# Kernel optimization log

Hardware: AMD Instinct MI355X
Metric: run time of the kernel (lower is better)

Reference implementation:

```python
import jax, jax.numpy as jnp
import numpy as np

B, Q, H, NH, HD = 2, 1024, 2048, 16, 128
QKV_ALPHA = 1e-4   # W8A8B8O8Linear output scale (a)
QKV_BETA = 1.0     # W8A8B8O8Linear bias scale (b)
QK_SCALE = 1e-4    # BMM_S8T_S8N_F32T dequant scale
PV_SCALE = 2e-3    # BMM_S8T_S8N_S8T output scale
DENSE_ALPHA = 1e-5 # W8A8BFP32OFP32Linear dequant scale
INV_NORM = 1.0 / (HD ** 0.5)


def setup_inputs() -> dict:
    key = jax.random.key(0)
    ks = jax.random.split(key, 8)
    hidden_states = jax.random.randint(ks[0], (B, Q, H), -128, 128, dtype=jnp.int32)  # int8 activations
    residual = jax.random.normal(ks[1], (B, Q, H), dtype=jnp.float32)
    alibi = jax.random.normal(ks[2], (B * NH, 1, Q), dtype=jnp.float32) * 0.1
    causal = jnp.triu(jnp.ones((Q, Q), dtype=bool), k=1)  # True = masked (future positions)
    attention_mask = jnp.broadcast_to(causal[None, None], (B, 1, Q, Q))
    w_qkv = jax.random.randint(ks[3], (3 * H, H), -128, 128, dtype=jnp.int32)   # int8 weight
    b_qkv = jax.random.randint(ks[4], (3 * H,), -128, 128, dtype=jnp.int32)     # int8 bias
    w_dense = jax.random.randint(ks[5], (H, H), -128, 128, dtype=jnp.int32)     # int8 weight
    b_dense = jax.random.normal(ks[6], (H,), dtype=jnp.float32)                 # fp32 bias
    return dict(hidden_states=hidden_states, residual=residual, alibi=alibi,
                attention_mask=attention_mask, w_qkv=w_qkv, b_qkv=b_qkv,
                w_dense=w_dense, b_dense=b_dense)


def _quant_i8(x_f32):
    return jnp.clip(jnp.round(x_f32), -128, 127).astype(jnp.int32)


def reference(hidden_states, residual, alibi, attention_mask, w_qkv, b_qkv, w_dense, b_dense):
    # --- W8A8B8O8 fused QKV linear: int8 in, int8 out ---
    acc = jnp.einsum('bqh,oh->bqo', hidden_states, w_qkv)  # exact int32 accumulation
    fused_qkv = _quant_i8(acc.astype(jnp.float32) * QKV_ALPHA + b_qkv.astype(jnp.float32) * QKV_BETA)
    # _split_heads: [B,Q,3H] -> [B,Q,NH,3,HD]
    qkv = fused_qkv.reshape(B, Q, NH, 3, HD)
    q = qkv[..., 0, :].transpose(0, 2, 1, 3).reshape(B * NH, Q, HD)
    k = qkv[..., 1, :].transpose(0, 2, 1, 3).reshape(B * NH, Q, HD)
    v = qkv[..., 2, :].transpose(0, 2, 1, 3).reshape(B * NH, Q, HD)
    # --- BMM_S8T_S8N_F32T: int8 q @ k^T -> fp32 * scale, plus alibi bias ---
    scores_i32 = jnp.einsum('nqd,nkd->nqk', q, k)  # [B*NH,Q,KV] int32
    matmul_result = alibi * 1.0 + scores_i32.astype(jnp.float32) * QK_SCALE * INV_NORM
    attention_scores = matmul_result.reshape(B, NH, Q, Q)
    # masked softmax (True = masked)
    attn_weights = jnp.where(attention_mask, jnp.finfo(jnp.float32).min, attention_scores)
    attention_probs = jax.nn.softmax(attn_weights, axis=-1)
    # quantize probs to int8 with scale 1/127 (BMM_S8T_S8N_S8T A-side)
    p_i8 = _quant_i8(attention_probs * 127.0).reshape(B * NH, Q, Q)
    # --- BMM_S8T_S8N_S8T: int8 probs @ int8 v -> int8 context ---
    ctx_acc = jnp.einsum('nqk,nkd->nqd', p_i8, v)  # int32
    ctx_i8 = _quant_i8(ctx_acc.astype(jnp.float32) * PV_SCALE)
    # _merge_heads: [B*NH,Q,HD] -> [B,Q,H]
    ctx = ctx_i8.reshape(B, NH, Q, HD).transpose(0, 2, 1, 3).reshape(B, Q, H)
    # --- W8A8BFP32OFP32 dense: int8 in, fp32 out ---
    dense_acc = jnp.einsum('bqh,oh->bqo', ctx, w_dense)
    output = dense_acc.astype(jnp.float32) * DENSE_ALPHA + b_dense + residual
    return output
```

## Files before the change

kernel.cpp:

```cpp
#include <hip/hip_runtime.h>
#include <stdint.h>

typedef int i32x4 __attribute__((ext_vector_type(4)));

#define DEV __device__ __forceinline__

DEV void glds16(const void* g, void* l) {
  __builtin_amdgcn_global_load_lds(
      (const __attribute__((address_space(1))) void*)g,
      (__attribute__((address_space(3))) void*)l, 16, 0, 0);
}

DEV int clampi8(float f) {
  int v = (int)rintf(f);
  return v < -128 ? -128 : (v > 127 ? 127 : v);
}

__global__ void pack_all_kernel(const int* __restrict__ s0, const int* __restrict__ s1,
                                const int* __restrict__ s2, int8_t* __restrict__ d0,
                                int8_t* __restrict__ d1, int8_t* __restrict__ d2) {
  const int i = blockIdx.x * 256 + threadIdx.x;
  const int* s;
  int8_t* d;
  int j;
  if (i < 1048576) { s = s0; d = d0; j = i; }
  else if (i < 4194304) { s = s1; d = d1; j = i - 1048576; }
  else { s = s2; d = d2; j = i - 4194304; }
  int4 v = ((const int4*)s)[j];
  char4 c;
  c.x = (char)v.x; c.y = (char)v.y; c.z = (char)v.z; c.w = (char)v.w;
  ((char4*)d)[j] = c;
}

template<int K>
DEV void gemm_core(const int8_t* __restrict__ A, const int8_t* __restrict__ B,
                   int row0, int col0, i32x4 acc[4][4], char* lA, char* lB,
                   int l, int w, int wm, int wn) {
  const int lr = l & 15, lg = l >> 4;
  const int8_t* pA0 = A + (size_t)(row0 + (w * 2 + 0) * 16 + lr) * K + lg * 16;
  const int8_t* pA1 = A + (size_t)(row0 + (w * 2 + 1) * 16 + lr) * K + lg * 16;
  const int8_t* pB0 = B + (size_t)(col0 + (w * 2 + 0) * 16 + lr) * K + lg * 16;
  const int8_t* pB1 = B + (size_t)(col0 + (w * 2 + 1) * 16 + lr) * K + lg * 16;
  glds16(pA0, lA + (w * 2 + 0) * 1024);
  glds16(pA1, lA + (w * 2 + 1) * 1024);
  glds16(pB0, lB + (w * 2 + 0) * 1024);
  glds16(pB1, lB + (w * 2 + 1) * 1024);
  __syncthreads();
  int cur = 0;
  for (int k0 = 0; k0 < K; k0 += 64) {
    const int nxt = cur ^ 1;
    if (k0 + 64 < K) {
      glds16(pA0 + k0 + 64, lA + nxt * 8192 + (w * 2 + 0) * 1024);
      glds16(pA1 + k0 + 64, lA + nxt * 8192 + (w * 2 + 1) * 1024);
      glds16(pB0 + k0 + 64, lB + nxt * 8192 + (w * 2 + 0) * 1024);
      glds16(pB1 + k0 + 64, lB + nxt * 8192 + (w * 2 + 1) * 1024);
    }
    i32x4 a[4], b[4];
#pragma unroll
    for (int i = 0; i < 4; ++i)
      a[i] = *(const i32x4*)(lA + cur * 8192 + ((wm * 4 + i) * 64 + l) * 16);
#pragma unroll
    for (int j = 0; j < 4; ++j)
      b[j] = *(const i32x4*)(lB + cur * 8192 + ((wn * 4 + j) * 64 + l) * 16);
#pragma unroll
    for (int i = 0; i < 4; ++i)
#pragma unroll
      for (int j = 0; j < 4; ++j)
        acc[i][j] = __builtin_amdgcn_mfma_i32_16x16x64_i8(a[i], b[j], acc[i][j], 0, 0, 0);
    __syncthreads();
    cur = nxt;
  }
}

__global__ __launch_bounds__(256) void qkv_kernel(
    const int8_t* __restrict__ hs8, const int8_t* __restrict__ w8,
    const int* __restrict__ bq, int8_t* __restrict__ qb, int8_t* __restrict__ kb,
    int8_t* __restrict__ vT) {
  __shared__ __align__(16) char lA[16384];
  __shared__ __align__(16) char lB[16384];
  const int l = threadIdx.x & 63, w = threadIdx.x >> 6;
  const int wm = w >> 1, wn = w & 1;
  const int lr = l & 15, lg = l >> 4;
  const int row0 = blockIdx.y * 128, col0 = blockIdx.x * 128;
  i32x4 acc[4][4] = {};
  gemm_core<2048>(hs8, w8, row0, col0, acc, lA, lB, l, w, wm, wn);
#pragma unroll
  for (int j = 0; j < 4; ++j) {
    const int col = col0 + (wn * 4 + j) * 16 + lr;
    const float bias = (float)bq[col];
    const int nh = col / 384, rem = col - nh * 384;
    const int s = rem >> 7, d = rem & 127;
#pragma unroll
    for (int i = 0; i < 4; ++i) {
#pragma unroll
      for (int r = 0; r < 4; ++r) {
        const int row = row0 + (wm * 4 + i) * 16 + lg * 4 + r;
        const int bb = row >> 10, qpos = row & 1023;
        const int n = bb * 16 + nh;
        const int8_t c = (int8_t)clampi8((float)acc[i][j][r] * 1e-4f + bias);
        if (s == 0)      qb[((size_t)n << 17) + (qpos << 7) + d] = c;
        else if (s == 1) kb[((size_t)n << 17) + (qpos << 7) + d] = c;
        else             vT[((size_t)n << 17) + (d << 10) + qpos] = c;
      }
    }
  }
}

__global__ __launch_bounds__(256) void attn_stats_kernel(
    const int8_t* __restrict__ qb, const int8_t* __restrict__ kb,
    const float* __restrict__ alibi, float* __restrict__ stats) {
  const int n = blockIdx.y;
  const int tri = blockIdx.x;
  int qt = 0;
  while ((qt + 1) * (qt + 2) / 2 <= tri) ++qt;
  const int kt = tri - qt * (qt + 1) / 2;
  const int l = threadIdx.x & 63, w = threadIdx.x >> 6;
  const int lr = l & 15, lg = l >> 4;
  const int row0 = qt * 128;
  const int8_t* Qh = qb + ((size_t)n << 17);
  const int8_t* Kh = kb + ((size_t)n << 17);
  const float* al = alibi + n * 1024;

  i32x4 qa[2][2];
#pragma unroll
  for (int t = 0; t < 2; ++t)
#pragma unroll
    for (int ks = 0; ks < 2; ++ks)
      qa[t][ks] = *(const i32x4*)(Qh + (size_t)(row0 + (w * 2 + t) * 16 + lr) * 128 + ks * 64 + lg * 16);

  float sf[2][8][4];
#pragma unroll
  for (int nf = 0; nf < 8; ++nf) {
    const size_t krow = (size_t)(kt * 128 + nf * 16 + lr) * 128;
    const i32x4 bk0 = *(const i32x4*)(Kh + krow + lg * 16);
    const i32x4 bk1 = *(const i32x4*)(Kh + krow + 64 + lg * 16);
    const int col = kt * 128 + nf * 16 + lr;
    const float av = al[col];
#pragma unroll
    for (int t = 0; t < 2; ++t) {
      i32x4 sa = {0, 0, 0, 0};
      sa = __builtin_amdgcn_mfma_i32_16x16x64_i8(qa[t][0], bk0, sa, 0, 0, 0);
      sa = __builtin_amdgcn_mfma_i32_16x16x64_i8(qa[t][1], bk1, sa, 0, 0, 0);
#pragma unroll
      for (int r = 0; r < 4; ++r) {
        const int rowg = row0 + (w * 2 + t) * 16 + lg * 4 + r;
        sf[t][nf][r] = (col <= rowg)
            ? av + ((float)sa[r] * 1e-4f) * 0.08838834764831843f
            : -INFINITY;
      }
    }
  }
#pragma unroll
  for (int t = 0; t < 2; ++t)
#pragma unroll
    for (int r = 0; r < 4; ++r) {
      float tm = sf[t][0][r];
#pragma unroll
      for (int nf = 1; nf < 8; ++nf) tm = fmaxf(tm, sf[t][nf][r]);
#pragma unroll
      for (int o = 1; o < 16; o <<= 1) tm = fmaxf(tm, __shfl_xor(tm, o));
      float es = 0.f;
#pragma unroll
      for (int nf = 0; nf < 8; ++nf) es += __expf(sf[t][nf][r] - tm);
#pragma unroll
      for (int o = 1; o < 16; o <<= 1) es += __shfl_xor(es, o);
      if (lr == 0) {
        const int rowl = (w * 2 + t) * 16 + lg * 4 + r;
        float2* st = (float2*)stats;
        st[((n * 8 + qt) * 8 + kt) * 128 + rowl] = make_float2(tm, es);
      }
    }
}

__global__ __launch_bounds__(256) void attn_pv_kernel(
    const int8_t* __restrict__ qb, const int8_t* __restrict__ kb,
    const int8_t* __restrict__ vT, const float* __restrict__ alibi,
    const float* __restrict__ stats, int* __restrict__ slab0,
    int* __restrict__ slab1, int8_t* __restrict__ ctx) {
  __shared__ __align__(16) char lK[16384];
  __shared__ __align__(16) char lV[16384];
  __shared__ __align__(16) char lP[128 * 144];
  const int n = blockIdx.y, gi = blockIdx.x;
  const int sched[12] = {0x407, 0x847, 0x406, 0x403, 0x746, 0x305,
                         0x635, 0x304, 0x302, 0x534, 0x201, 0x100};
  const int s_ = sched[gi];
  const int qt = s_ & 15, kt0 = (s_ >> 4) & 15, kt1 = (s_ >> 8) & 15;
  const int l = threadIdx.x & 63, w = threadIdx.x >> 6;
  const int lr = l & 15, lg = l >> 4;
  const int row0 = qt * 128;
  const int8_t* Qh = qb + ((size_t)n << 17);
  const int8_t* Kh = kb + ((size_t)n << 17);
  const int8_t* Vh = vT + ((size_t)n << 17);
  const float* al = alibi + n * 1024;

  i32x4 qa[2][2];
#pragma unroll
  for (int t = 0; t < 2; ++t)
#pragma unroll
    for (int ks = 0; ks < 2; ++ks)
      qa[t][ks] = *(const i32x4*)(Qh + (size_t)(row0 + (w * 2 + t) * 16 + lr) * 128 + ks * 64 + lg * 16);

  float mrow[2][4], srow[2][4];
  const float2* st = (const float2*)stats;
#pragma unroll
  for (int t = 0; t < 2; ++t)
#pragma unroll
    for (int r = 0; r < 4; ++r) {
      const int rowl = (w * 2 + t) * 16 + lg * 4 + r;
      const int base = ((n * 8 + qt) * 8) * 128 + rowl;
      float m = -INFINITY;
      for (int k2 = 0; k2 <= qt; ++k2) m = fmaxf(m, st[base + k2 * 128].x);
      float s = 0.f;
      for (int k2 = 0; k2 <= qt; ++k2) {
        const float2 p = st[base + k2 * 128];
        s += p.y * __expf(p.x - m);
      }
      mrow[t][r] = m; srow[t][r] = s;
    }

  i32x4 pacc[2][8] = {};
  for (int kt = kt0; kt < kt1; ++kt) {
    __syncthreads();
#pragma unroll
    for (int e0 = 0; e0 < 4; ++e0) {
      const int e = w * 4 + e0, ks = e >> 3, mb = e & 7;
      glds16(Kh + (size_t)(kt * 128 + mb * 16 + lr) * 128 + ks * 64 + lg * 16, lK + e * 1024);
      glds16(Vh + (size_t)(mb * 16 + lr) * 1024 + kt * 128 + ks * 64 + lg * 16, lV + e * 1024);
    }
    __syncthreads();
#pragma unroll
    for (int nf = 0; nf < 8; ++nf) {
      const i32x4 bk0 = *(const i32x4*)(lK + nf * 1024 + l * 16);
      const i32x4 bk1 = *(const i32x4*)(lK + (8 + nf) * 1024 + l * 16);
      const int col = kt * 128 + nf * 16 + lr;
      const float av = al[col];
#pragma unroll
      for (int t = 0; t < 2; ++t) {
        i32x4 sa = {0, 0, 0, 0};
        sa = __builtin_amdgcn_mfma_i32_16x16x64_i8(qa[t][0], bk0, sa, 0, 0, 0);
        sa = __builtin_amdgcn_mfma_i32_16x16x64_i8(qa[t][1], bk1, sa, 0, 0, 0);
#pragma unroll
        for (int r = 0; r < 4; ++r) {
          const int rowl = (w * 2 + t) * 16 + lg * 4 + r;
          const int rowg = row0 + rowl;
          int p = 0;
          if (col <= rowg) {
            const float s = av + ((float)sa[r] * 1e-4f) * 0.08838834764831843f;
            p = (int)rintf(__expf(s - mrow[t][r]) / srow[t][r] * 127.0f);
          }
          lP[rowl * 144 + nf * 16 + lr] = (char)p;
        }
      }
    }
#pragma unroll
    for (int t = 0; t < 2; ++t) {
      const int rowl = (w * 2 + t) * 16 + lr;
      const i32x4 pa0 = *(const i32x4*)(lP + rowl * 144 + lg * 16);
      const i32x4 pa1 = *(const i32x4*)(lP + rowl * 144 + 64 + lg * 16);
#pragma unroll
      for (int nf = 0; nf < 8; ++nf) {
        const i32x4 vb0 = *(const i32x4*)(lV + nf * 1024 + l * 16);
        const i32x4 vb1 = *(const i32x4*)(lV + (8 + nf) * 1024 + l * 16);
        pacc[t][nf] = __builtin_amdgcn_mfma_i32_16x16x64_i8(pa0, vb0, pacc[t][nf], 0, 0, 0);
        pacc[t][nf] = __builtin_amdgcn_mfma_i32_16x16x64_i8(pa1, vb1, pacc[t][nf], 0, 0, 0);
      }
    }
  }
  const int bb = n >> 4, nh = n & 15;
  if (qt < 4) {
#pragma unroll
    for (int t = 0; t < 2; ++t)
#pragma unroll
      for (int nf = 0; nf < 8; ++nf)
#pragma unroll
        for (int r = 0; r < 4; ++r) {
          const int qpos = row0 + (w * 2 + t) * 16 + lg * 4 + r;
          const int d = nf * 16 + lr;
          ctx[((size_t)(bb * 1024 + qpos)) * 2048 + nh * 128 + d] =
              (int8_t)clampi8((float)pacc[t][nf][r] * 2e-3f);
        }
  } else {
    int* slab = kt0 ? slab1 : slab0;
#pragma unroll
    for (int t = 0; t < 2; ++t)
#pragma unroll
      for (int nf = 0; nf < 8; ++nf)
#pragma unroll
        for (int r = 0; r < 4; ++r) {
          const int qpos = row0 + (w * 2 + t) * 16 + lg * 4 + r;
          const int d = nf * 16 + lr;
          slab[(size_t)(bb * 512 + qpos - 512) * 2048 + nh * 128 + d] = pacc[t][nf][r];
        }
  }
}

__global__ void ctx_reduce_kernel(const int* __restrict__ slab0,
                                  const int* __restrict__ slab1,
                                  int8_t* __restrict__ ctx) {
  const int i = blockIdx.x * blockDim.x + threadIdx.x;
  const int4 a = ((const int4*)slab0)[i];
  const int4 b = ((const int4*)slab1)[i];
  const int elem0 = i * 4;
  const int r512 = elem0 >> 11, col = elem0 & 2047;
  const int bb = r512 >> 9, qpos = 512 + (r512 & 511);
  char4 c;
  c.x = (char)clampi8((float)(a.x + b.x) * 2e-3f);
  c.y = (char)clampi8((float)(a.y + b.y) * 2e-3f);
  c.z = (char)clampi8((float)(a.z + b.z) * 2e-3f);
  c.w = (char)clampi8((float)(a.w + b.w) * 2e-3f);
  ((char4*)ctx)[((size_t)(bb * 1024 + qpos) * 2048 + col) >> 2] = c;
}

__global__ __launch_bounds__(512, 1) void dense_kernel(
    const int8_t* __restrict__ c8, const int8_t* __restrict__ w8,
    const float* __restrict__ bd, const float* __restrict__ res,
    float* __restrict__ out) {
  __shared__ __align__(16) char lA[16384];
  __shared__ __align__(16) char lB[16384];
  const int l = threadIdx.x & 63, w = threadIdx.x >> 6;
  const int wm = w >> 2, wn = w & 3;
  const int lr = l & 15, lg = l >> 4;
  const int row0 = blockIdx.y * 128, col0 = blockIdx.x * 128;
  const int8_t* pA = c8 + (size_t)(row0 + w * 16 + lr) * 2048 + lg * 16;
  const int8_t* pB = w8 + (size_t)(col0 + w * 16 + lr) * 2048 + lg * 16;
  glds16(pA, lA + w * 1024);
  glds16(pB, lB + w * 1024);
  __syncthreads();
  i32x4 acc[4][2] = {};
  int cur = 0;
  for (int k0 = 0; k0 < 2048; k0 += 64) {
    const int nxt = cur ^ 1;
    if (k0 + 64 < 2048) {
      glds16(pA + k0 + 64, lA + nxt * 8192 + w * 1024);
      glds16(pB + k0 + 64, lB + nxt * 8192 + w * 1024);
    }
    i32x4 a[4], b[2];
#pragma unroll
    for (int i = 0; i < 4; ++i)
      a[i] = *(const i32x4*)(lA + cur * 8192 + ((wm * 4 + i) * 64 + l) * 16);
#pragma unroll
    for (int j = 0; j < 2; ++j)
      b[j] = *(const i32x4*)(lB + cur * 8192 + ((wn * 2 + j) * 64 + l) * 16);
#pragma unroll
    for (int i = 0; i < 4; ++i)
#pragma unroll
      for (int j = 0; j < 2; ++j)
        acc[i][j] = __builtin_amdgcn_mfma_i32_16x16x64_i8(a[i], b[j], acc[i][j], 0, 0, 0);
    __syncthreads();
    cur = nxt;
  }
#pragma unroll
  for (int j = 0; j < 2; ++j) {
    const int col = col0 + (wn * 2 + j) * 16 + lr;
    const float bias = bd[col];
#pragma unroll
    for (int i = 0; i < 4; ++i) {
#pragma unroll
      for (int r = 0; r < 4; ++r) {
        const int row = row0 + (wm * 4 + i) * 16 + lg * 4 + r;
        const size_t o = (size_t)row * 2048 + col;
        out[o] = (float)acc[i][j][r] * 1e-5f + bias + res[o];
      }
    }
  }
}

extern "C" void kernel_launch(void* const* d_in, const int* in_sizes, int n_in,
                              void* d_out, int out_size, void* d_ws, size_t ws_size,
                              hipStream_t stream) {
  const int* hs = (const int*)d_in[0];
  const float* res = (const float*)d_in[1];
  const float* alibi = (const float*)d_in[2];
  const int* wqkv = (const int*)d_in[4];
  const int* bqkv = (const int*)d_in[5];
  const int* wd = (const int*)d_in[6];
  const float* bd = (const float*)d_in[7];
  float* out = (float*)d_out;
  char* ws = (char*)d_ws;

  int8_t* hs8   = (int8_t*)(ws + 0);
  int8_t* wqkv8 = (int8_t*)(ws + 4194304);
  int*    slab0 = (int*)(ws + 0);
  int*    slab1 = (int*)(ws + 8388608);
  int8_t* wd8   = (int8_t*)(ws + 16777216);
  int8_t* q8b   = (int8_t*)(ws + 20971520);
  int8_t* k8b   = (int8_t*)(ws + 25165824);
  int8_t* vT8   = (int8_t*)(ws + 29360128);
  int8_t* ctx8  = (int8_t*)(ws + 33554432);
  float*  stats = (float*)(ws + 37748736);

  pack_all_kernel<<<20480, 256, 0, stream>>>(hs, wqkv, wd, hs8, wqkv8, wd8);
  qkv_kernel<<<dim3(48, 16), 256, 0, stream>>>(hs8, wqkv8, bqkv, q8b, k8b, vT8);
  attn_stats_kernel<<<dim3(36, 32), 256, 0, stream>>>(q8b, k8b, alibi, stats);
  attn_pv_kernel<<<dim3(12, 32), 256, 0, stream>>>(q8b, k8b, vT8, alibi, stats,
                                                   slab0, slab1, ctx8);
  ctx_reduce_kernel<<<2048, 256, 0, stream>>>(slab0, slab1, ctx8);
  dense_kernel<<<dim3(16, 16), 512, 0, stream>>>(ctx8, wd8, bd, res, out);
}
```

Measured before the change: 178.3 us.

## Load QKV GEMM operands directly into registers instead of staging through LDS

The QKV projection GEMM no longer stages A and B tiles through shared memory with global_load_lds. Each wave now loads its own MFMA fragments straight from global memory into registers, double-buffered across K steps. This removes the LDS writes and reads and the per-iteration __syncthreads barriers. In exchange, waves that share rows or columns of the tile load the same data separately, which adds cache traffic. The loads are also less coalesced, at 64-byte row segments.

```diff
diff --git a/kernel.cpp b/kernel.cpp
--- a/kernel.cpp
+++ b/kernel.cpp
@@ -32,58 +32,45 @@
   ((char4*)d)[j] = c;
 }
 
-template<int K>
-DEV void gemm_core(const int8_t* __restrict__ A, const int8_t* __restrict__ B,
-                   int row0, int col0, i32x4 acc[4][4], char* lA, char* lB,
-                   int l, int w, int wm, int wn) {
-  const int lr = l & 15, lg = l >> 4;
-  const int8_t* pA0 = A + (size_t)(row0 + (w * 2 + 0) * 16 + lr) * K + lg * 16;
-  const int8_t* pA1 = A + (size_t)(row0 + (w * 2 + 1) * 16 + lr) * K + lg * 16;
-  const int8_t* pB0 = B + (size_t)(col0 + (w * 2 + 0) * 16 + lr) * K + lg * 16;
-  const int8_t* pB1 = B + (size_t)(col0 + (w * 2 + 1) * 16 + lr) * K + lg * 16;
-  glds16(pA0, lA + (w * 2 + 0) * 1024);
-  glds16(pA1, lA + (w * 2 + 1) * 1024);
-  glds16(pB0, lB + (w * 2 + 0) * 1024);
-  glds16(pB1, lB + (w * 2 + 1) * 1024);
-  __syncthreads();
-  int cur = 0;
-  for (int k0 = 0; k0 < K; k0 += 64) {
-    const int nxt = cur ^ 1;
-    if (k0 + 64 < K) {
-      glds16(pA0 + k0 + 64, lA + nxt * 8192 + (w * 2 + 0) * 1024);
-      glds16(pA1 + k0 + 64, lA + nxt * 8192 + (w * 2 + 1) * 1024);
-      glds16(pB0 + k0 + 64, lB + nxt * 8192 + (w * 2 + 0) * 1024);
-      glds16(pB1 + k0 + 64, lB + nxt * 8192 + (w * 2 + 1) * 1024);
-    }
-    i32x4 a[4], b[4];
-#pragma unroll
-    for (int i = 0; i < 4; ++i)
-      a[i] = *(const i32x4*)(lA + cur * 8192 + ((wm * 4 + i) * 64 + l) * 16);
-#pragma unroll
-    for (int j = 0; j < 4; ++j)
-      b[j] = *(const i32x4*)(lB + cur * 8192 + ((wn * 4 + j) * 64 + l) * 16);
-#pragma unroll
-    for (int i = 0; i < 4; ++i)
-#pragma unroll
-      for (int j = 0; j < 4; ++j)
-        acc[i][j] = __builtin_amdgcn_mfma_i32_16x16x64_i8(a[i], b[j], acc[i][j], 0, 0, 0);
-    __syncthreads();
-    cur = nxt;
-  }
-}
-
 __global__ __launch_bounds__(256) void qkv_kernel(
     const int8_t* __restrict__ hs8, const int8_t* __restrict__ w8,
     const int* __restrict__ bq, int8_t* __restrict__ qb, int8_t* __restrict__ kb,
     int8_t* __restrict__ vT) {
-  __shared__ __align__(16) char lA[16384];
-  __shared__ __align__(16) char lB[16384];
   const int l = threadIdx.x & 63, w = threadIdx.x >> 6;
   const int wm = w >> 1, wn = w & 1;
   const int lr = l & 15, lg = l >> 4;
   const int row0 = blockIdx.y * 128, col0 = blockIdx.x * 128;
+  const int8_t* pA[4];
+  const int8_t* pB[4];
+#pragma unroll
+  for (int i = 0; i < 4; ++i)
+    pA[i] = hs8 + (size_t)(row0 + (wm * 4 + i) * 16 + lr) * 2048 + lg * 16;
+#pragma unroll
+  for (int j = 0; j < 4; ++j)
+    pB[j] = w8 + (size_t)(col0 + (wn * 4 + j) * 16 + lr) * 2048 + lg * 16;
   i32x4 acc[4][4] = {};
-  gemm_core<2048>(hs8, w8, row0, col0, acc, lA, lB, l, w, wm, wn);
+  i32x4 a[4], b[4], an[4], bn[4];
+#pragma unroll
+  for (int i = 0; i < 4; ++i) a[i] = *(const i32x4*)(pA[i]);
+#pragma unroll
+  for (int j = 0; j < 4; ++j) b[j] = *(const i32x4*)(pB[j]);
+  for (int k0 = 0; k0 < 2048; k0 += 64) {
+    if (k0 + 64 < 2048) {
+#pragma unroll
+      for (int i = 0; i < 4; ++i) an[i] = *(const i32x4*)(pA[i] + k0 + 64);
+#pragma unroll
+      for (int j = 0; j < 4; ++j) bn[j] = *(const i32x4*)(pB[j] + k0 + 64);
+    }
+#pragma unroll
+    for (int i = 0; i < 4; ++i)
+#pragma unroll
+      for (int j = 0; j < 4; ++j)
+        acc[i][j] = __builtin_amdgcn_mfma_i32_16x16x64_i8(a[i], b[j], acc[i][j], 0, 0, 0);
+#pragma unroll
+    for (int i = 0; i < 4; ++i) a[i] = an[i];
+#pragma unroll
+    for (int j = 0; j < 4; ++j) b[j] = bn[j];
+  }
 #pragma unroll
   for (int j = 0; j < 4; ++j) {
     const int col = col0 + (wn * 4 + j) * 16 + lr;
```

After: 251.8 us. 41.2% more time.
